# Kernel tuning notes

Measured on AMD Instinct MI355X. Metric: run time of the kernel, lower is better.

The kernel has to match this reference:

```python
import jax, jax.numpy as jnp
import numpy as np


def setup_inputs() -> dict:
    key = jax.random.key(0)
    k1, k2, k3 = jax.random.split(key, 3)
    B, K, IN, OUT = 4096, 8, 1024, 1024
    x = jax.random.normal(k1, (B, IN), dtype=jnp.float32)
    blend_weights = jax.random.uniform(k2, (B, K), dtype=jnp.float32)
    weight = jax.random.normal(k3, (K, OUT, IN), dtype=jnp.float32) * 0.01
    bias = jnp.zeros((K, OUT), dtype=jnp.float32)
    return {"x": x, "blend_weights": blend_weights, "weight": weight, "bias": bias}


def reference(x, blend_weights, weight, bias):
    # Mathematically identical to blending weights first then matvec:
    #   einsum('bk,koi->boi') then bmm  ==  per-expert GEMM then blend.
    # per-expert outputs: (b, k, o)
    expert_out = jnp.einsum('bi,koi->bko', x, weight)
    out = jnp.einsum('bk,bko->bo', blend_weights, expert_out)
    out = out + blend_weights @ bias  # (b,k) @ (k,o) -> (b,o)
    return out
```

## Files before the change

### kernel.cpp

```cpp
#include <hip/hip_runtime.h>
#include <hip/hip_bf16.h>
#include <stdint.h>

typedef short short8 __attribute__((ext_vector_type(8)));
typedef float f32x4  __attribute__((ext_vector_type(4)));
typedef unsigned short u16;

#define B_ROWS 4096
#define NEXP   8
#define IN_D   1024
#define OUT_D  1024

__device__ __forceinline__ u16 f2bf(float f) {
    uint32_t u = __float_as_uint(f);
    uint32_t r = (u + 0x7fffu + ((u >> 16) & 1u)) >> 16;
    return (u16)r;
}

#define W_CVT_BLOCKS 8192
__global__ __launch_bounds__(256) void prep(const float* __restrict__ x,
                                            const float* __restrict__ bwt,
                                            const float* __restrict__ wgt,
                                            u16* __restrict__ ab,
                                            u16* __restrict__ wb) {
    const int bid = blockIdx.x;
    if (bid < W_CVT_BLOCKS) {
        const int i = bid * 256 + threadIdx.x;
        float4 v = reinterpret_cast<const float4*>(wgt)[i];
        ushort4 o;
        o.x = f2bf(v.x); o.y = f2bf(v.y); o.z = f2bf(v.z); o.w = f2bf(v.w);
        reinterpret_cast<ushort4*>(wb)[i] = o;
    } else {
        const int b = bid - W_CVT_BLOCKS;
        const int i4 = threadIdx.x;
        float4 v = reinterpret_cast<const float4*>(x)[(size_t)b * 256 + i4];
        float4 w0 = reinterpret_cast<const float4*>(bwt)[b * 2];
        float4 w1 = reinterpret_cast<const float4*>(bwt)[b * 2 + 1];
        float wk[8] = {w0.x, w0.y, w0.z, w0.w, w1.x, w1.y, w1.z, w1.w};
        #pragma unroll
        for (int k = 0; k < NEXP; ++k) {
            ushort4 o;
            o.x = f2bf(wk[k] * v.x); o.y = f2bf(wk[k] * v.y);
            o.z = f2bf(wk[k] * v.z); o.w = f2bf(wk[k] * v.w);
            reinterpret_cast<ushort4*>(ab)[((size_t)k * B_ROWS + b) * 256 + i4] = o;
        }
    }
}

__device__ __forceinline__ void glds16(const u16* g, u16* lds_base, uint32_t off) {
    auto gp = (const __attribute__((address_space(1))) void*)(uintptr_t)(g);
    auto lp = (__attribute__((address_space(3))) void*)(uintptr_t)((const char*)lds_base + off);
    __builtin_amdgcn_global_load_lds(gp, lp, 16, 0, 0);
}

#define PHASE(BUF, QM, QN, LOADA, STAGE_STMT)                                     \
  {                                                                               \
    asm volatile("s_waitcnt vmcnt(6)" ::: "memory");                              \
    if (LOADA) {                                                                  \
      _Pragma("unroll") for (int mi = 0; mi < 4; ++mi)                            \
        _Pragma("unroll") for (int ks = 0; ks < 2; ++ks)                          \
          af[mi][ks] = *(const short8*)(ldsc + (BUF)*65536 + (QM)*16384 +         \
                                        aRowB + mi*2048 + cXor[ks]);              \
    }                                                                             \
    _Pragma("unroll") for (int ni = 0; ni < 2; ++ni)                              \
      _Pragma("unroll") for (int ks = 0; ks < 2; ++ks)                            \
        bf[ni][ks] = *(const short8*)(ldsc + (BUF)*65536 + 32768 + (QN)*16384 +   \
                                      bRowB + ni*2048 + cXor[ks]);                \
    STAGE_STMT;                                                                   \
    __builtin_amdgcn_s_barrier();                                                 \
    __builtin_amdgcn_s_setprio(1);                                                \
    _Pragma("unroll") for (int mi = 0; mi < 4; ++mi)                              \
      _Pragma("unroll") for (int ni = 0; ni < 2; ++ni) {                          \
        acc[QM][QN][mi][ni] = __builtin_amdgcn_mfma_f32_16x16x32_bf16(            \
            af[mi][0], bf[ni][0], acc[QM][QN][mi][ni], 0, 0, 0);                  \
        acc[QM][QN][mi][ni] = __builtin_amdgcn_mfma_f32_16x16x32_bf16(            \
            af[mi][1], bf[ni][1], acc[QM][QN][mi][ni], 0, 0, 0);                  \
      }                                                                           \
    __builtin_amdgcn_s_setprio(0);                                                \
    __builtin_amdgcn_s_barrier();                                                 \
  }

__global__ __launch_bounds__(512, 2) void moe_gemm8(
    const u16* __restrict__ Ab,
    const u16* __restrict__ Wb,
    float* __restrict__ parts,
    float* __restrict__ out,
    int epb, int nz)
{
    __shared__ __align__(16) u16 lds[65536];

    const int nwg = gridDim.x;
    const int cpx = nwg >> 3;
    const int id  = blockIdx.x;
    const int swz = (id & 7) * cpx + (id >> 3);
    const int bz  = swz >> 6;
    const int rem = swz & 63;
    const int bm_g = (rem >> 2) * 256;
    const int bn_g = (rem & 3) * 256;

    const int tid  = threadIdx.x;
    const int lane = tid & 63, wid = tid >> 6;
    const int wm = wid >> 2, wn = wid & 3;
    const int lr = lane & 15, lg = lane >> 4;

    const int nt   = epb << 4;
    const int ntm1 = nt - 1;
    const int nit  = nt >> 1;

    const int row0   = wid * 8 + (lane >> 3);
    const int colOff = ((lane & 7) ^ (lane >> 3)) * 8;

    const char* ldsc = (const char*)lds;
    const int aRowB = (wm * 64 + lr) * 128;
    const int bRowB = (wn * 32 + lr) * 128;
    int cXor[2];
    cXor[0] = (lg * 16) ^ ((lr & 7) << 4);
    cXor[1] = (64 + lg * 16) ^ ((lr & 7) << 4);

    auto STAGE = [&](int t, int isB, int h, int buf) {
        const int kexp = bz * epb + (t >> 4);
        const int i0 = (t & 15) << 6;
        const u16* gp = isB
            ? Wb + ((size_t)kexp * OUT_D + bn_g + h * 128 + row0) * IN_D + i0 + colOff
            : Ab + ((size_t)kexp * B_ROWS + bm_g + h * 128 + row0) * IN_D + i0 + colOff;
        const uint32_t l0 = (uint32_t)((buf << 16) + (isB << 15) + (h << 14) + (wid << 10));
        glds16(gp, lds, l0);
        glds16(gp + (size_t)64 * IN_D, lds, l0 + 8192);
    };

    f32x4 acc[2][2][4][2];
    #pragma unroll
    for (int a = 0; a < 2; ++a)
      #pragma unroll
      for (int b = 0; b < 2; ++b)
        #pragma unroll
        for (int c = 0; c < 4; ++c)
          #pragma unroll
          for (int d = 0; d < 2; ++d)
            acc[a][b][c][d] = (f32x4){0.f, 0.f, 0.f, 0.f};

    short8 af[4][2], bf[2][2];

    STAGE(0, 0, 0, 0);
    STAGE(0, 1, 0, 0);
    STAGE(0, 1, 1, 0);
    STAGE(0, 0, 1, 0);
    STAGE(1, 0, 0, 1);
    STAGE(1, 1, 0, 1);
    asm volatile("s_waitcnt vmcnt(0)" ::: "memory");
    __builtin_amdgcn_s_barrier();

    for (int m = 0; m < nit; ++m) {
        const int t1 = 2 * m + 1;
        const int t2 = (t1 + 1) & ntm1;
        const int t3 = (t1 + 2) & ntm1;
        PHASE(0, 0, 0, 1, STAGE(t1, 1, 1, 1));
        PHASE(0, 0, 1, 0, STAGE(t1, 0, 1, 1));
        PHASE(0, 1, 0, 1, STAGE(t2, 0, 0, 0));
        PHASE(0, 1, 1, 0, STAGE(t2, 1, 0, 0));
        PHASE(1, 0, 0, 1, STAGE(t2, 1, 1, 0));
        PHASE(1, 0, 1, 0, STAGE(t2, 0, 1, 0));
        PHASE(1, 1, 0, 1, STAGE(t3, 0, 0, 1));
        PHASE(1, 1, 1, 0, STAGE(t3, 1, 0, 1));
    }

    float* op = (bz == nz - 1) ? out : parts + (size_t)bz * B_ROWS * OUT_D;
    #pragma unroll
    for (int qm = 0; qm < 2; ++qm)
      #pragma unroll
      for (int mi = 0; mi < 4; ++mi)
        #pragma unroll
        for (int qn = 0; qn < 2; ++qn)
          #pragma unroll
          for (int ni = 0; ni < 2; ++ni)
            #pragma unroll
            for (int r = 0; r < 4; ++r) {
                const int grow = bm_g + qm * 128 + wm * 64 + mi * 16 + lg * 4 + r;
                const int gcol = bn_g + qn * 128 + wn * 32 + ni * 16 + lr;
                op[(size_t)grow * OUT_D + gcol] = acc[qm][qn][mi][ni][r];
            }
}

__global__ __launch_bounds__(256) void reduce_bias(
    const float* __restrict__ parts, const float* __restrict__ bwt,
    const float* __restrict__ bias, float* __restrict__ out, int np)
{
    const int i4 = blockIdx.x * 256 + threadIdx.x;
    const size_t total = (size_t)B_ROWS * OUT_D;
    const size_t base = (size_t)i4 * 4;
    if (base >= total) return;
    const int brow = (int)(base >> 10);
    const int o = (int)(base & 1023);

    float4 s = *reinterpret_cast<const float4*>(out + base);
    for (int z = 0; z < np; ++z) {
        float4 p = *reinterpret_cast<const float4*>(parts + (size_t)z * total + base);
        s.x += p.x; s.y += p.y; s.z += p.z; s.w += p.w;
    }
    #pragma unroll
    for (int k = 0; k < NEXP; ++k) {
        const float w = bwt[brow * NEXP + k];
        float4 bb = *reinterpret_cast<const float4*>(bias + k * OUT_D + o);
        s.x += w * bb.x; s.y += w * bb.y; s.z += w * bb.z; s.w += w * bb.w;
    }
    *reinterpret_cast<float4*>(out + base) = s;
}

__global__ __launch_bounds__(256) void naive_moe(
    const float* __restrict__ x, const float* __restrict__ bwt,
    const float* __restrict__ wgt, const float* __restrict__ bias,
    float* __restrict__ out)
{
    __shared__ float xs[IN_D];
    const int brow = blockIdx.x;
    const int o = blockIdx.y * 256 + threadIdx.x;
    for (int i = threadIdx.x; i < IN_D; i += 256) xs[i] = x[(size_t)brow * IN_D + i];
    __syncthreads();
    float acc = 0.f;
    for (int k = 0; k < NEXP; ++k) {
        const float* wr = wgt + ((size_t)k * OUT_D + o) * IN_D;
        float d = 0.f;
        for (int i = 0; i < IN_D; ++i) d += xs[i] * wr[i];
        acc += bwt[brow * NEXP + k] * (d + bias[k * OUT_D + o]);
    }
    out[(size_t)brow * OUT_D + o] = acc;
}

extern "C" void kernel_launch(void* const* d_in, const int* in_sizes, int n_in,
                              void* d_out, int out_size, void* d_ws, size_t ws_size,
                              hipStream_t stream) {
    const float* x    = (const float*)d_in[0];
    const float* bwt  = (const float*)d_in[1];
    const float* wgt  = (const float*)d_in[2];
    const float* bias = (const float*)d_in[3];
    float* out = (float*)d_out;

    const size_t a_bytes    = (size_t)NEXP * B_ROWS * IN_D * 2;
    const size_t w_bytes    = (size_t)NEXP * OUT_D * IN_D * 2;
    const size_t part_bytes = (size_t)B_ROWS * OUT_D * 4;

    if (ws_size < a_bytes + w_bytes) {
        naive_moe<<<dim3(B_ROWS, OUT_D / 256), 256, 0, stream>>>(x, bwt, wgt, bias, out);
        return;
    }

    int nz = 1;
    if      (ws_size >= a_bytes + w_bytes + 3 * part_bytes) nz = 4;
    else if (ws_size >= a_bytes + w_bytes + 1 * part_bytes) nz = 2;

    u16* ab = (u16*)d_ws;
    u16* wb = (u16*)((char*)d_ws + a_bytes);
    float* parts = (float*)((char*)d_ws + a_bytes + w_bytes);

    prep<<<W_CVT_BLOCKS + B_ROWS, 256, 0, stream>>>(x, bwt, wgt, ab, wb);

    moe_gemm8<<<64 * nz, 512, 0, stream>>>(ab, wb, parts, out, NEXP / nz, nz);

    reduce_bias<<<(B_ROWS * OUT_D / 4 + 255) / 256, 256, 0, stream>>>(
        parts, bwt, bias, out, nz - 1);
}
```

Baseline: 184.6 us.

## Apply blend weights by accumulator rescaling instead of materializing per-expert scaled inputs

```diff
diff --git a/kernel.cpp b/kernel.cpp
--- a/kernel.cpp
+++ b/kernel.cpp
@@ -16,12 +16,14 @@
     uint32_t r = (u + 0x7fffu + ((u >> 16) & 1u)) >> 16;
     return (u16)r;
 }
+__device__ __forceinline__ float bf2f(u16 h) {
+    return __uint_as_float((uint32_t)h << 16);
+}
 
 #define W_CVT_BLOCKS 8192
 __global__ __launch_bounds__(256) void prep(const float* __restrict__ x,
-                                            const float* __restrict__ bwt,
                                             const float* __restrict__ wgt,
-                                            u16* __restrict__ ab,
+                                            u16* __restrict__ xb,
                                             u16* __restrict__ wb) {
     const int bid = blockIdx.x;
     if (bid < W_CVT_BLOCKS) {
@@ -31,18 +33,14 @@
         o.x = f2bf(v.x); o.y = f2bf(v.y); o.z = f2bf(v.z); o.w = f2bf(v.w);
         reinterpret_cast<ushort4*>(wb)[i] = o;
     } else {
-        const int b = bid - W_CVT_BLOCKS;
-        const int i4 = threadIdx.x;
-        float4 v = reinterpret_cast<const float4*>(x)[(size_t)b * 256 + i4];
-        float4 w0 = reinterpret_cast<const float4*>(bwt)[b * 2];
-        float4 w1 = reinterpret_cast<const float4*>(bwt)[b * 2 + 1];
-        float wk[8] = {w0.x, w0.y, w0.z, w0.w, w1.x, w1.y, w1.z, w1.w};
+        const int base = (bid - W_CVT_BLOCKS) * 256 + threadIdx.x;
         #pragma unroll
-        for (int k = 0; k < NEXP; ++k) {
+        for (int j = 0; j < 4; ++j) {
+            const int i = base + j * 262144;
+            float4 v = reinterpret_cast<const float4*>(x)[i];
             ushort4 o;
-            o.x = f2bf(wk[k] * v.x); o.y = f2bf(wk[k] * v.y);
-            o.z = f2bf(wk[k] * v.z); o.w = f2bf(wk[k] * v.w);
-            reinterpret_cast<ushort4*>(ab)[((size_t)k * B_ROWS + b) * 256 + i4] = o;
+            o.x = f2bf(v.x); o.y = f2bf(v.y); o.z = f2bf(v.z); o.w = f2bf(v.w);
+            reinterpret_cast<ushort4*>(xb)[i] = o;
         }
     }
 }
@@ -81,9 +79,10 @@
   }
 
 __global__ __launch_bounds__(512, 2) void moe_gemm8(
-    const u16* __restrict__ Ab,
+    const u16* __restrict__ Xb,
     const u16* __restrict__ Wb,
-    float* __restrict__ parts,
+    const float* __restrict__ bwt,
+    u16* __restrict__ parts,
     float* __restrict__ out,
     int epb, int nz)
 {
@@ -105,7 +104,6 @@
 
     const int nt   = epb << 4;
     const int ntm1 = nt - 1;
-    const int nit  = nt >> 1;
 
     const int row0   = wid * 8 + (lane >> 3);
     const int colOff = ((lane & 7) ^ (lane >> 3)) * 8;
@@ -122,7 +120,7 @@
         const int i0 = (t & 15) << 6;
         const u16* gp = isB
             ? Wb + ((size_t)kexp * OUT_D + bn_g + h * 128 + row0) * IN_D + i0 + colOff
-            : Ab + ((size_t)kexp * B_ROWS + bm_g + h * 128 + row0) * IN_D + i0 + colOff;
+            : Xb + (size_t)(bm_g + h * 128 + row0) * IN_D + i0 + colOff;
         const uint32_t l0 = (uint32_t)((buf << 16) + (isB << 15) + (h << 14) + (wid << 10));
         glds16(gp, lds, l0);
         glds16(gp + (size_t)64 * IN_D, lds, l0 + 8192);
@@ -150,39 +148,67 @@
     asm volatile("s_waitcnt vmcnt(0)" ::: "memory");
     __builtin_amdgcn_s_barrier();
 
-    for (int m = 0; m < nit; ++m) {
-        const int t1 = 2 * m + 1;
-        const int t2 = (t1 + 1) & ntm1;
-        const int t3 = (t1 + 2) & ntm1;
-        PHASE(0, 0, 0, 1, STAGE(t1, 1, 1, 1));
-        PHASE(0, 0, 1, 0, STAGE(t1, 0, 1, 1));
-        PHASE(0, 1, 0, 1, STAGE(t2, 0, 0, 0));
-        PHASE(0, 1, 1, 0, STAGE(t2, 1, 0, 0));
-        PHASE(1, 0, 0, 1, STAGE(t2, 1, 1, 0));
-        PHASE(1, 0, 1, 0, STAGE(t2, 0, 1, 0));
-        PHASE(1, 1, 0, 1, STAGE(t3, 0, 0, 1));
-        PHASE(1, 1, 1, 0, STAGE(t3, 1, 0, 1));
-    }
-
-    float* op = (bz == nz - 1) ? out : parts + (size_t)bz * B_ROWS * OUT_D;
+    int m = 0;
+    for (int e = 0; e < epb; ++e) {
+        if (e) {
+            const int kprev = bz * epb + e - 1;
+            #pragma unroll
+            for (int qm = 0; qm < 2; ++qm)
+              #pragma unroll
+              for (int mi = 0; mi < 4; ++mi)
+                #pragma unroll
+                for (int r = 0; r < 4; ++r) {
+                    const int grow = bm_g + qm * 128 + wm * 64 + mi * 16 + lg * 4 + r;
+                    const float cp = fmaxf(bwt[grow * NEXP + kprev], 1e-20f);
+                    const float cc = fmaxf(bwt[grow * NEXP + kprev + 1], 1e-20f);
+                    const float rr = cp / cc;
+                    #pragma unroll
+                    for (int qn = 0; qn < 2; ++qn)
+                      #pragma unroll
+                      for (int ni = 0; ni < 2; ++ni)
+                          acc[qm][qn][mi][ni][r] *= rr;
+                }
+        }
+        for (int s = 0; s < 8; ++s, ++m) {
+            const int t1 = 2 * m + 1;
+            const int t2 = (t1 + 1) & ntm1;
+            const int t3 = (t1 + 2) & ntm1;
+            PHASE(0, 0, 0, 1, STAGE(t1, 1, 1, 1));
+            PHASE(0, 0, 1, 0, STAGE(t1, 0, 1, 1));
+            PHASE(0, 1, 0, 1, STAGE(t2, 0, 0, 0));
+            PHASE(0, 1, 1, 0, STAGE(t2, 1, 0, 0));
+            PHASE(1, 0, 0, 1, STAGE(t2, 1, 1, 0));
+            PHASE(1, 0, 1, 0, STAGE(t2, 0, 1, 0));
+            PHASE(1, 1, 0, 1, STAGE(t3, 0, 0, 1));
+            PHASE(1, 1, 1, 0, STAGE(t3, 1, 0, 1));
+        }
+    }
+
+    const int klast = bz * epb + epb - 1;
+    const bool last_slice = (bz == nz - 1);
+    u16* pp = parts + (size_t)bz * B_ROWS * OUT_D;
     #pragma unroll
     for (int qm = 0; qm < 2; ++qm)
       #pragma unroll
       for (int mi = 0; mi < 4; ++mi)
         #pragma unroll
-        for (int qn = 0; qn < 2; ++qn)
-          #pragma unroll
-          for (int ni = 0; ni < 2; ++ni)
+        for (int r = 0; r < 4; ++r) {
+            const int grow = bm_g + qm * 128 + wm * 64 + mi * 16 + lg * 4 + r;
+            const float cl = fmaxf(bwt[grow * NEXP + klast], 1e-20f);
             #pragma unroll
-            for (int r = 0; r < 4; ++r) {
-                const int grow = bm_g + qm * 128 + wm * 64 + mi * 16 + lg * 4 + r;
-                const int gcol = bn_g + qn * 128 + wn * 32 + ni * 16 + lr;
-                op[(size_t)grow * OUT_D + gcol] = acc[qm][qn][mi][ni][r];
-            }
+            for (int qn = 0; qn < 2; ++qn)
+              #pragma unroll
+              for (int ni = 0; ni < 2; ++ni) {
+                  const int gcol = bn_g + qn * 128 + wn * 32 + ni * 16 + lr;
+                  const float v = acc[qm][qn][mi][ni][r] * cl;
+                  if (last_slice) out[(size_t)grow * OUT_D + gcol] = v;
+                  else            pp[(size_t)grow * OUT_D + gcol] = f2bf(v);
+              }
+        }
 }
 
 __global__ __launch_bounds__(256) void reduce_bias(
-    const float* __restrict__ parts, const float* __restrict__ bwt,
+    const u16* __restrict__ parts, const float* __restrict__ bwt,
     const float* __restrict__ bias, float* __restrict__ out, int np)
 {
     const int i4 = blockIdx.x * 256 + threadIdx.x;
@@ -194,8 +220,8 @@
 
     float4 s = *reinterpret_cast<const float4*>(out + base);
     for (int z = 0; z < np; ++z) {
-        float4 p = *reinterpret_cast<const float4*>(parts + (size_t)z * total + base);
-        s.x += p.x; s.y += p.y; s.z += p.z; s.w += p.w;
+        ushort4 p = *reinterpret_cast<const ushort4*>(parts + (size_t)z * total + base);
+        s.x += bf2f(p.x); s.y += bf2f(p.y); s.z += bf2f(p.z); s.w += bf2f(p.w);
     }
     #pragma unroll
     for (int k = 0; k < NEXP; ++k) {
@@ -235,26 +261,26 @@
     const float* bias = (const float*)d_in[3];
     float* out = (float*)d_out;
 
-    const size_t a_bytes    = (size_t)NEXP * B_ROWS * IN_D * 2;
+    const size_t x_bytes    = (size_t)B_ROWS * IN_D * 2;
     const size_t w_bytes    = (size_t)NEXP * OUT_D * IN_D * 2;
-    const size_t part_bytes = (size_t)B_ROWS * OUT_D * 4;
-
-    if (ws_size < a_bytes + w_bytes) {
+    const size_t part_bytes = (size_t)B_ROWS * OUT_D * 2;
+
+    if (ws_size < x_bytes + w_bytes) {
         naive_moe<<<dim3(B_ROWS, OUT_D / 256), 256, 0, stream>>>(x, bwt, wgt, bias, out);
         return;
     }
 
     int nz = 1;
-    if      (ws_size >= a_bytes + w_bytes + 3 * part_bytes) nz = 4;
-    else if (ws_size >= a_bytes + w_bytes + 1 * part_bytes) nz = 2;
-
-    u16* ab = (u16*)d_ws;
-    u16* wb = (u16*)((char*)d_ws + a_bytes);
-    float* parts = (float*)((char*)d_ws + a_bytes + w_bytes);
-
-    prep<<<W_CVT_BLOCKS + B_ROWS, 256, 0, stream>>>(x, bwt, wgt, ab, wb);
-
-    moe_gemm8<<<64 * nz, 512, 0, stream>>>(ab, wb, parts, out, NEXP / nz, nz);
+    if      (ws_size >= x_bytes + w_bytes + 3 * part_bytes) nz = 4;
+    else if (ws_size >= x_bytes + w_bytes + 1 * part_bytes) nz = 2;
+
+    u16* xb = (u16*)d_ws;
+    u16* wb = (u16*)((char*)d_ws + x_bytes);
+    u16* parts = (u16*)((char*)d_ws + x_bytes + w_bytes);
+
+    prep<<<W_CVT_BLOCKS + 1024, 256, 0, stream>>>(x, wgt, xb, wb);
+
+    moe_gemm8<<<64 * nz, 512, 0, stream>>>(xb, wb, bwt, parts, out, NEXP / nz, nz);
 
     reduce_bias<<<(B_ROWS * OUT_D / 4 + 255) / 256, 256, 0, stream>>>(
         parts, bwt, bias, out, nz - 1);
```

Result: no change. 181.5 us (-1.7%).

## Shrink GEMM tile to 256x128 and fix expert split at two partials

Applied to the files above, without the earlier changes.

```diff
diff --git a/kernel.cpp b/kernel.cpp
--- a/kernel.cpp
+++ b/kernel.cpp
@@ -53,50 +53,50 @@
     __builtin_amdgcn_global_load_lds(gp, lp, 16, 0, 0);
 }
 
-#define PHASE(BUF, QM, QN, LOADA, STAGE_STMT)                                     \
+#define PHASE(BUF, QM, LOADB, STAGE_STMT)                                         \
   {                                                                               \
     asm volatile("s_waitcnt vmcnt(6)" ::: "memory");                              \
-    if (LOADA) {                                                                  \
-      _Pragma("unroll") for (int mi = 0; mi < 4; ++mi)                            \
+    _Pragma("unroll") for (int mi = 0; mi < 4; ++mi)                              \
+      _Pragma("unroll") for (int ks = 0; ks < 2; ++ks)                            \
+        af[mi][ks] = *(const short8*)(ldsc + (BUF)*49152 + (QM)*16384 +           \
+                                      aRowB + mi*2048 + cXor[ks]);                \
+    if (LOADB) {                                                                  \
+      _Pragma("unroll") for (int ni = 0; ni < 2; ++ni)                            \
         _Pragma("unroll") for (int ks = 0; ks < 2; ++ks)                          \
-          af[mi][ks] = *(const short8*)(ldsc + (BUF)*65536 + (QM)*16384 +         \
-                                        aRowB + mi*2048 + cXor[ks]);              \
+          bf[ni][ks] = *(const short8*)(ldsc + (BUF)*49152 + 32768 +              \
+                                        bRowB + ni*2048 + cXor[ks]);              \
     }                                                                             \
-    _Pragma("unroll") for (int ni = 0; ni < 2; ++ni)                              \
-      _Pragma("unroll") for (int ks = 0; ks < 2; ++ks)                            \
-        bf[ni][ks] = *(const short8*)(ldsc + (BUF)*65536 + 32768 + (QN)*16384 +   \
-                                      bRowB + ni*2048 + cXor[ks]);                \
     STAGE_STMT;                                                                   \
     __builtin_amdgcn_s_barrier();                                                 \
     __builtin_amdgcn_s_setprio(1);                                                \
     _Pragma("unroll") for (int mi = 0; mi < 4; ++mi)                              \
       _Pragma("unroll") for (int ni = 0; ni < 2; ++ni) {                          \
-        acc[QM][QN][mi][ni] = __builtin_amdgcn_mfma_f32_16x16x32_bf16(            \
-            af[mi][0], bf[ni][0], acc[QM][QN][mi][ni], 0, 0, 0);                  \
-        acc[QM][QN][mi][ni] = __builtin_amdgcn_mfma_f32_16x16x32_bf16(            \
-            af[mi][1], bf[ni][1], acc[QM][QN][mi][ni], 0, 0, 0);                  \
+        acc[QM][mi][ni] = __builtin_amdgcn_mfma_f32_16x16x32_bf16(                \
+            af[mi][0], bf[ni][0], acc[QM][mi][ni], 0, 0, 0);                      \
+        acc[QM][mi][ni] = __builtin_amdgcn_mfma_f32_16x16x32_bf16(                \
+            af[mi][1], bf[ni][1], acc[QM][mi][ni], 0, 0, 0);                      \
       }                                                                           \
     __builtin_amdgcn_s_setprio(0);                                                \
     __builtin_amdgcn_s_barrier();                                                 \
   }
 
-__global__ __launch_bounds__(512, 2) void moe_gemm8(
+__global__ __launch_bounds__(512, 2) void moe_gemm4p(
     const u16* __restrict__ Ab,
     const u16* __restrict__ Wb,
     float* __restrict__ parts,
     float* __restrict__ out,
-    int epb, int nz)
+    int epb)
 {
-    __shared__ __align__(16) u16 lds[65536];
+    __shared__ __align__(16) u16 lds[49152];
 
     const int nwg = gridDim.x;
     const int cpx = nwg >> 3;
     const int id  = blockIdx.x;
     const int swz = (id & 7) * cpx + (id >> 3);
-    const int bz  = swz >> 6;
-    const int rem = swz & 63;
-    const int bm_g = (rem >> 2) * 256;
-    const int bn_g = (rem & 3) * 256;
+    const int bz  = swz >> 7;
+    const int rem = swz & 127;
+    const int bm_g = (rem >> 3) * 256;
+    const int bn_g = (rem & 7) * 128;
 
     const int tid  = threadIdx.x;
     const int lane = tid & 63, wid = tid >> 6;
@@ -121,30 +121,27 @@
         const int kexp = bz * epb + (t >> 4);
         const int i0 = (t & 15) << 6;
         const u16* gp = isB
-            ? Wb + ((size_t)kexp * OUT_D + bn_g + h * 128 + row0) * IN_D + i0 + colOff
+            ? Wb + ((size_t)kexp * OUT_D + bn_g + row0) * IN_D + i0 + colOff
             : Ab + ((size_t)kexp * B_ROWS + bm_g + h * 128 + row0) * IN_D + i0 + colOff;
-        const uint32_t l0 = (uint32_t)((buf << 16) + (isB << 15) + (h << 14) + (wid << 10));
+        const uint32_t l0 = (uint32_t)(buf * 49152 + (isB ? 32768 : h * 16384) + (wid << 10));
         glds16(gp, lds, l0);
         glds16(gp + (size_t)64 * IN_D, lds, l0 + 8192);
     };
 
-    f32x4 acc[2][2][4][2];
+    f32x4 acc[2][4][2];
     #pragma unroll
     for (int a = 0; a < 2; ++a)
       #pragma unroll
-      for (int b = 0; b < 2; ++b)
+      for (int c = 0; c < 4; ++c)
         #pragma unroll
-        for (int c = 0; c < 4; ++c)
-          #pragma unroll
-          for (int d = 0; d < 2; ++d)
-            acc[a][b][c][d] = (f32x4){0.f, 0.f, 0.f, 0.f};
+        for (int d = 0; d < 2; ++d)
+          acc[a][c][d] = (f32x4){0.f, 0.f, 0.f, 0.f};
 
     short8 af[4][2], bf[2][2];
 
     STAGE(0, 0, 0, 0);
+    STAGE(0, 0, 1, 0);
     STAGE(0, 1, 0, 0);
-    STAGE(0, 1, 1, 0);
-    STAGE(0, 0, 1, 0);
     STAGE(1, 0, 0, 1);
     STAGE(1, 1, 0, 1);
     asm volatile("s_waitcnt vmcnt(0)" ::: "memory");
@@ -154,36 +151,30 @@
         const int t1 = 2 * m + 1;
         const int t2 = (t1 + 1) & ntm1;
         const int t3 = (t1 + 2) & ntm1;
-        PHASE(0, 0, 0, 1, STAGE(t1, 1, 1, 1));
-        PHASE(0, 0, 1, 0, STAGE(t1, 0, 1, 1));
-        PHASE(0, 1, 0, 1, STAGE(t2, 0, 0, 0));
-        PHASE(0, 1, 1, 0, STAGE(t2, 1, 0, 0));
-        PHASE(1, 0, 0, 1, STAGE(t2, 1, 1, 0));
-        PHASE(1, 0, 1, 0, STAGE(t2, 0, 1, 0));
-        PHASE(1, 1, 0, 1, STAGE(t3, 0, 0, 1));
-        PHASE(1, 1, 1, 0, STAGE(t3, 1, 0, 1));
-    }
-
-    float* op = (bz == nz - 1) ? out : parts + (size_t)bz * B_ROWS * OUT_D;
+        PHASE(0, 0, 1, STAGE(t1, 0, 1, 1));
+        PHASE(0, 1, 0, { STAGE(t2, 0, 0, 0); STAGE(t2, 1, 0, 0); });
+        PHASE(1, 0, 1, STAGE(t2, 0, 1, 0));
+        PHASE(1, 1, 0, { STAGE(t3, 0, 0, 1); STAGE(t3, 1, 0, 1); });
+    }
+
+    float* op = (bz == 1) ? out : parts;
     #pragma unroll
     for (int qm = 0; qm < 2; ++qm)
       #pragma unroll
       for (int mi = 0; mi < 4; ++mi)
         #pragma unroll
-        for (int qn = 0; qn < 2; ++qn)
+        for (int ni = 0; ni < 2; ++ni)
           #pragma unroll
-          for (int ni = 0; ni < 2; ++ni)
-            #pragma unroll
-            for (int r = 0; r < 4; ++r) {
-                const int grow = bm_g + qm * 128 + wm * 64 + mi * 16 + lg * 4 + r;
-                const int gcol = bn_g + qn * 128 + wn * 32 + ni * 16 + lr;
-                op[(size_t)grow * OUT_D + gcol] = acc[qm][qn][mi][ni][r];
-            }
+          for (int r = 0; r < 4; ++r) {
+              const int grow = bm_g + qm * 128 + wm * 64 + mi * 16 + lg * 4 + r;
+              const int gcol = bn_g + wn * 32 + ni * 16 + lr;
+              op[(size_t)grow * OUT_D + gcol] = acc[qm][mi][ni][r];
+          }
 }
 
 __global__ __launch_bounds__(256) void reduce_bias(
     const float* __restrict__ parts, const float* __restrict__ bwt,
-    const float* __restrict__ bias, float* __restrict__ out, int np)
+    const float* __restrict__ bias, float* __restrict__ out)
 {
     const int i4 = blockIdx.x * 256 + threadIdx.x;
     const size_t total = (size_t)B_ROWS * OUT_D;
@@ -193,10 +184,8 @@
     const int o = (int)(base & 1023);
 
     float4 s = *reinterpret_cast<const float4*>(out + base);
-    for (int z = 0; z < np; ++z) {
-        float4 p = *reinterpret_cast<const float4*>(parts + (size_t)z * total + base);
-        s.x += p.x; s.y += p.y; s.z += p.z; s.w += p.w;
-    }
+    float4 p = *reinterpret_cast<const float4*>(parts + base);
+    s.x += p.x; s.y += p.y; s.z += p.z; s.w += p.w;
     #pragma unroll
     for (int k = 0; k < NEXP; ++k) {
         const float w = bwt[brow * NEXP + k];
@@ -239,14 +228,10 @@
     const size_t w_bytes    = (size_t)NEXP * OUT_D * IN_D * 2;
     const size_t part_bytes = (size_t)B_ROWS * OUT_D * 4;
 
-    if (ws_size < a_bytes + w_bytes) {
+    if (ws_size < a_bytes + w_bytes + part_bytes) {
         naive_moe<<<dim3(B_ROWS, OUT_D / 256), 256, 0, stream>>>(x, bwt, wgt, bias, out);
         return;
     }
-
-    int nz = 1;
-    if      (ws_size >= a_bytes + w_bytes + 3 * part_bytes) nz = 4;
-    else if (ws_size >= a_bytes + w_bytes + 1 * part_bytes) nz = 2;
 
     u16* ab = (u16*)d_ws;
     u16* wb = (u16*)((char*)d_ws + a_bytes);
@@ -254,8 +239,8 @@
 
     prep<<<W_CVT_BLOCKS + B_ROWS, 256, 0, stream>>>(x, bwt, wgt, ab, wb);
 
-    moe_gemm8<<<64 * nz, 512, 0, stream>>>(ab, wb, parts, out, NEXP / nz, nz);
+    moe_gemm4p<<<256, 512, 0, stream>>>(ab, wb, parts, out, NEXP / 2);
 
     reduce_bias<<<(B_ROWS * OUT_D / 4 + 255) / 256, 256, 0, stream>>>(
-        parts, bwt, bias, out, nz - 1);
-}
+        parts, bwt, bias, out);
+}
```

Result: no change. 181.4 us (-1.7%).
